# Kernel optimization log

Measured on AMD Instinct MI355X. Metric: run time of the kernel, lower is better.

The kernel has to match this reference:

```python
import jax, jax.numpy as jnp
import numpy as np

COS_EPS = 1e-6      # torch CosineSimilarity eps
NORM_EPS = 1e-12    # F.normalize default eps
NUM_HEADS = 4
TOPK = 5


def setup_inputs() -> dict:
    key = jax.random.key(0)
    ks = jax.random.split(key, 12)
    B, S, D_in, D = 32, 256, 768, 1024
    N = 50000
    sc = 0.02
    return {
        "hidden": jax.random.normal(ks[0], (B, S, D_in), jnp.float32),
        "table": jax.random.normal(ks[1], (N, D), jnp.float32),
        "fc1_w": jax.random.normal(ks[2], (D, D_in), jnp.float32) * sc,
        "fc1_b": jax.random.normal(ks[3], (D,), jnp.float32) * sc,
        "q_w": jax.random.normal(ks[4], (D, D), jnp.float32) * sc,
        "q_b": jax.random.normal(ks[5], (D,), jnp.float32) * sc,
        "k_w": jax.random.normal(ks[6], (D, D), jnp.float32) * sc,
        "k_b": jax.random.normal(ks[7], (D,), jnp.float32) * sc,
        "v_w": jax.random.normal(ks[8], (D, D), jnp.float32) * sc,
        "v_b": jax.random.normal(ks[9], (D,), jnp.float32) * sc,
        "out_w": jax.random.normal(ks[10], (D, D), jnp.float32) * sc,
        "out_b": jax.random.normal(ks[11], (D,), jnp.float32) * sc,
    }


def reference(hidden, table, fc1_w, fc1_b, q_w, q_b, k_w, k_b, v_w, v_b, out_w, out_b):
    B, S, _ = hidden.shape
    D = fc1_w.shape[0]
    H = NUM_HEADS
    hd = D // H

    # fc1 over last BERT hidden states: [B,S,1024]
    x = jnp.einsum("bsi,di->bsd", hidden, fc1_w) + fc1_b

    # ---- per-sample retrieval (vectorized over batch) ----
    m = jnp.mean(x, axis=1)                       # [B,D] mean over seq
    tn = jnp.linalg.norm(table, axis=1)           # [N]
    mn = jnp.linalg.norm(m, axis=1)               # [B]
    sim = (m @ table.T) / (jnp.maximum(mn, COS_EPS)[:, None]
                           * jnp.maximum(tn, COS_EPS)[None, :])  # [B,N]
    best = jnp.argmax(sim, axis=1)                # [B] top-1 cosine match

    tab_n = table / jnp.maximum(tn, NORM_EPS)[:, None]  # L2-normalized table
    sel = tab_n[best]                             # [B,D]
    # squared euclidean distance, expanded form (avoids [B,N,D] intermediate)
    d2 = (jnp.sum(sel * sel, axis=1)[:, None]
          - 2.0 * (sel @ tab_n.T)
          + jnp.sum(tab_n * tab_n, axis=1)[None, :])  # [B,N]
    _, idx = jax.lax.top_k(-d2, TOPK)             # 5 smallest distances
    targets = table[idx]                          # [B,5,D] (unnormalized rows)

    # ---- torch.nn.MultiheadAttention(query=targets, key=x, value=x) ----
    q = (jnp.einsum("bqd,ed->bqe", targets, q_w) + q_b).reshape(B, TOPK, H, hd)
    k = (jnp.einsum("bsd,ed->bse", x, k_w) + k_b).reshape(B, S, H, hd)
    v = (jnp.einsum("bsd,ed->bse", x, v_w) + v_b).reshape(B, S, H, hd)
    scores = jnp.einsum("bqhd,bkhd->bhqk", q, k) / jnp.sqrt(jnp.asarray(hd, x.dtype))
    attn = jax.nn.softmax(scores, axis=-1)        # [B,H,5,S]
    o = jnp.einsum("bhqk,bkhd->bqhd", attn, v).reshape(B, TOPK, D)
    attn_out = jnp.einsum("bqe,de->bqd", o, out_w) + out_b  # [B,5,D]

    return jnp.sum(attn_out, axis=1)              # [B,D]
```

## Files before the change

### kernel.cpp

```cpp
#include <hip/hip_runtime.h>
#include <stdint.h>

typedef short bf16x8 __attribute__((ext_vector_type(8)));
typedef float f32x4 __attribute__((ext_vector_type(4)));

#define NROWS 50000
#define BATCH 32
#define SEQ 256
#define DIN 768
#define DMODEL 1024
#define NTOPK 5
#define DOTS_BLOCKS 782
#define CHUNKF 64
#define NCHUNK (DMODEL / CHUNKF)

__device__ inline unsigned short f2bf(float f) {
  union { float f; unsigned u; } x; x.f = f;
  unsigned u = x.u;
  unsigned r = u + 0x7fffu + ((u >> 16) & 1u);
  return (unsigned short)(r >> 16);
}
__device__ inline float bf2f(unsigned short h) {
  union { unsigned u; float f; } x; x.u = ((unsigned)h) << 16; return x.f;
}

__device__ __forceinline__ void gl_lds16(const void* g, void* l) {
  __builtin_amdgcn_global_load_lds(
      (const __attribute__((address_space(1))) unsigned int*)g,
      (__attribute__((address_space(3))) unsigned int*)l, 16, 0, 0);
}

__global__ void k_f32_to_bf16(const float* __restrict__ in, unsigned short* __restrict__ out, int n) {
  int i = (blockIdx.x * blockDim.x + threadIdx.x) * 4;
  int stride = gridDim.x * blockDim.x * 4;
  for (; i < n; i += stride) {
    float4 f = *(const float4*)(in + i);
    ushort4 o;
    o.x = f2bf(f.x); o.y = f2bf(f.y); o.z = f2bf(f.z); o.w = f2bf(f.w);
    *(ushort4*)(out + i) = o;
  }
}

__global__ void k_f32_to_bf16_3(const float* __restrict__ i0, unsigned short* __restrict__ o0, int n0,
                                const float* __restrict__ i1, unsigned short* __restrict__ o1, int n1,
                                const float* __restrict__ i2, unsigned short* __restrict__ o2, int n2) {
  int base = (blockIdx.x * blockDim.x + threadIdx.x) * 4;
  int stride = gridDim.x * blockDim.x * 4;
  for (int i = base; i < n0; i += stride) {
    float4 f = *(const float4*)(i0 + i);
    ushort4 o; o.x = f2bf(f.x); o.y = f2bf(f.y); o.z = f2bf(f.z); o.w = f2bf(f.w);
    *(ushort4*)(o0 + i) = o;
  }
  for (int i = base; i < n1; i += stride) {
    float4 f = *(const float4*)(i1 + i);
    ushort4 o; o.x = f2bf(f.x); o.y = f2bf(f.y); o.z = f2bf(f.z); o.w = f2bf(f.w);
    *(ushort4*)(o1 + i) = o;
  }
  for (int i = base; i < n2; i += stride) {
    float4 f = *(const float4*)(i2 + i);
    ushort4 o; o.x = f2bf(f.x); o.y = f2bf(f.y); o.z = f2bf(f.z); o.w = f2bf(f.w);
    *(ushort4*)(o2 + i) = o;
  }
}

__global__ void k_mean_part(const float* __restrict__ hidden, float* __restrict__ hpart) {
  int b = blockIdx.x >> 3, tc = blockIdx.x & 7;
  int i = threadIdx.x;
  const float* p = hidden + ((size_t)b * SEQ + tc * 32) * DIN + i;
  float s = 0.f;
  #pragma unroll 4
  for (int t = 0; t < 32; ++t) s += p[t * DIN];
  hpart[((size_t)tc * 32 + b) * DIN + i] = s;
}
__global__ void k_mean_reduce(const float* __restrict__ hpart, float* __restrict__ hm) {
  int b = blockIdx.x;
  int i = threadIdx.x;
  float s = 0.f;
  #pragma unroll
  for (int tc = 0; tc < 8; ++tc) s += hpart[((size_t)tc * 32 + b) * DIN + i];
  hm[b * DIN + i] = s * (1.0f / SEQ);
}

__global__ void k_sgemm_wt(const float* __restrict__ A, const float* __restrict__ W,
                           const float* __restrict__ bias, float* __restrict__ C,
                           int M, int N, int K, float beta) {
  __shared__ float A_l[32][65];
  __shared__ float W_l[64][65];
  int tid = threadIdx.x;
  int tx = tid & 63, ty = tid >> 6;
  int n0 = blockIdx.x * 64, m0 = blockIdx.y * 32;
  float acc[8] = {0.f,0.f,0.f,0.f,0.f,0.f,0.f,0.f};
  for (int k0 = 0; k0 < K; k0 += 64) {
    #pragma unroll
    for (int i = 0; i < 8; ++i) {
      int idx = tid + 256 * i; int r = idx >> 6, c = idx & 63;
      A_l[r][c] = A[(size_t)(m0 + r) * K + k0 + c];
    }
    #pragma unroll
    for (int i = 0; i < 16; ++i) {
      int idx = tid + 256 * i; int r = idx >> 6, c = idx & 63;
      W_l[r][c] = W[(size_t)(n0 + r) * K + k0 + c];
    }
    __syncthreads();
    for (int kk = 0; kk < 64; ++kk) {
      float wv = W_l[tx][kk];
      #pragma unroll
      for (int r = 0; r < 8; ++r) acc[r] += A_l[ty * 8 + r][kk] * wv;
    }
    __syncthreads();
  }
  float bv = bias[n0 + tx] * beta;
  #pragma unroll
  for (int r = 0; r < 8; ++r) C[(size_t)(m0 + ty * 8 + r) * N + n0 + tx] = acc[r] + bv;
}

__global__ __launch_bounds__(256) void k_bf16_gemm(const unsigned short* __restrict__ A,
    const unsigned short* __restrict__ W, const float* __restrict__ bias,
    unsigned short* __restrict__ C, int M, int N, int K) {
  __shared__ unsigned short As[128][32];
  __shared__ unsigned short Ws[128][32];
  int tid = threadIdx.x;
  int wave = tid >> 6, lane = tid & 63;
  int wr = wave >> 1, wc = wave & 1;
  int bm = blockIdx.y * 128, bn = blockIdx.x * 128;
  int srow = lane >> 2;
  int scol = (lane & 3) * 8;
  f32x4 acc[4][4] = {};
  for (int k0 = 0; k0 < K; k0 += 32) {
    #pragma unroll
    for (int j = 0; j < 2; ++j) {
      int r0 = wave * 32 + j * 16;
      gl_lds16(A + (size_t)(bm + r0 + srow) * K + k0 + scol, &As[r0][0]);
      gl_lds16(W + (size_t)(bn + r0 + srow) * K + k0 + scol, &Ws[r0][0]);
    }
    __syncthreads();
    bf16x8 af[4], bfr[4];
    #pragma unroll
    for (int mi = 0; mi < 4; ++mi)
      af[mi] = *(const bf16x8*)(&As[wr * 64 + mi * 16 + (lane & 15)][(lane >> 4) * 8]);
    #pragma unroll
    for (int ni = 0; ni < 4; ++ni)
      bfr[ni] = *(const bf16x8*)(&Ws[wc * 64 + ni * 16 + (lane & 15)][(lane >> 4) * 8]);
    #pragma unroll
    for (int mi = 0; mi < 4; ++mi)
      #pragma unroll
      for (int ni = 0; ni < 4; ++ni)
        acc[mi][ni] = __builtin_amdgcn_mfma_f32_16x16x32_bf16(af[mi], bfr[ni], acc[mi][ni], 0, 0, 0);
    __syncthreads();
  }
  #pragma unroll
  for (int ni = 0; ni < 4; ++ni) {
    int col = bn + wc * 64 + ni * 16 + (lane & 15);
    float bv = bias[col];
    #pragma unroll
    for (int mi = 0; mi < 4; ++mi) {
      #pragma unroll
      for (int j = 0; j < 4; ++j) {
        int row = bm + wr * 64 + mi * 16 + (lane >> 4) * 4 + j;
        C[(size_t)row * N + col] = f2bf(acc[mi][ni][j] + bv);
      }
    }
  }
}

__global__ __launch_bounds__(256, 4) void k_dots(const float* __restrict__ table,
    const float* __restrict__ vecs, float* __restrict__ norm2g,
    float* __restrict__ candv, int* __restrict__ candi, int pass1, float eps) {
  __shared__ float t_lds[2][64 * 64];
  __shared__ float norm_lds[64];
  __shared__ float iv_lds[64];
  float* dot_lds = &t_lds[0][0];

  int tid = threadIdx.x;
  int wave = tid >> 6, lane = tid & 63;
  int rbase = blockIdx.x * 64;

  int b0 = __builtin_amdgcn_readfirstlane(wave * 8);
  const float* qb = vecs + (size_t)b0 * DMODEL;

  int u = lane & 15;
  int rsub = lane >> 4;

  float acc[8] = {0.f,0.f,0.f,0.f,0.f,0.f,0.f,0.f};
  float accn = 0.f;

  auto STAGE = [&](int buf, int k0) {
    #pragma unroll
    for (int j = 0; j < 4; ++j) {
      int rl = wave * 16 + j * 4 + rsub;
      int gr = rbase + rl; if (gr >= NROWS) gr = NROWS - 1;
      int c = ((u & 7) ^ (rl & 7)) | (u & 8);
      gl_lds16(table + (size_t)gr * DMODEL + k0 + c * 4,
               &t_lds[buf][(wave * 16 + j * 4) * 64]);
    }
  };

  STAGE(0, 0);
  __syncthreads();
  int cur = 0;
  for (int ch = 0; ch < NCHUNK; ++ch) {
    int k0 = ch * CHUNKF;
    if (ch + 1 < NCHUNK) STAGE(cur ^ 1, k0 + CHUNKF);
    #pragma unroll 2
    for (int q4 = 0; q4 < 16; ++q4) {
      int uu = ((q4 & 7) ^ (lane & 7)) | (q4 & 8);
      float4 tv = *(const float4*)(&t_lds[cur][lane * 64 + uu * 4]);
      if (pass1 && wave == 0)
        accn += tv.x * tv.x + tv.y * tv.y + tv.z * tv.z + tv.w * tv.w;
      #pragma unroll
      for (int j = 0; j < 8; ++j) {
        float4 qv = *(const float4*)(qb + (size_t)j * DMODEL + k0 + q4 * 4);
        acc[j] += tv.x * qv.x + tv.y * qv.y + tv.z * qv.z + tv.w * qv.w;
      }
    }
    __syncthreads();
    cur ^= 1;
  }

  #pragma unroll
  for (int j = 0; j < 8; ++j) dot_lds[(wave * 8 + j) * 66 + lane] = acc[j];
  if (wave == 0) {
    norm_lds[lane] = accn;
    if (pass1) {
      int rw = rbase + lane;
      if (rw < NROWS) norm2g[rw] = accn;
    }
  }
  __syncthreads();
  if (tid < 64) {
    int rc = rbase + tid;
    if (rc >= NROWS) rc = NROWS - 1;
    float n2 = pass1 ? norm_lds[tid] : norm2g[rc];
    iv_lds[tid] = 1.0f / fmaxf(sqrtf(n2), eps);
  }
  __syncthreads();

  if (tid < 32) {
    float tv[5]; int ti[5];
    #pragma unroll
    for (int j = 0; j < 5; ++j) { tv[j] = -3.4e38f; ti[j] = 0x7fffffff; }
    for (int r = 0; r < 64; ++r) {
      int rw = rbase + r;
      if (rw >= NROWS) break;
      float v = dot_lds[tid * 66 + r] * iv_lds[r];
      if (v > tv[4] || (v == tv[4] && rw < ti[4])) {
        tv[4] = v; ti[4] = rw;
        #pragma unroll
        for (int j = 4; j > 0; --j) {
          bool sw = (tv[j] > tv[j-1]) || (tv[j] == tv[j-1] && ti[j] < ti[j-1]);
          if (sw) {
            float fv = tv[j]; tv[j] = tv[j-1]; tv[j-1] = fv;
            int ivx = ti[j]; ti[j] = ti[j-1]; ti[j-1] = ivx;
          }
        }
      }
    }
    #pragma unroll
    for (int j = 0; j < 5; ++j) {
      candv[((size_t)blockIdx.x * 32 + tid) * 5 + j] = tv[j];
      candi[((size_t)blockIdx.x * 32 + tid) * 5 + j] = ti[j];
    }
  }
}

__global__ void k_merge(const float* __restrict__ candv, const int* __restrict__ candi,
                        int* __restrict__ out_idx, int K, int nblk) {
  int b = blockIdx.x;
  int tid = threadIdx.x;
  float tv[5]; int ti[5];
  #pragma unroll
  for (int j = 0; j < 5; ++j) { tv[j] = -3.4e38f; ti[j] = 0x7fffffff; }
  for (int blk = tid; blk < nblk; blk += 256) {
    #pragma unroll
    for (int j = 0; j < 5; ++j) {
      float v = candv[((size_t)blk * 32 + b) * 5 + j];
      int idx = candi[((size_t)blk * 32 + b) * 5 + j];
      if (v > tv[4] || (v == tv[4] && idx < ti[4])) {
        tv[4] = v; ti[4] = idx;
        #pragma unroll
        for (int jj = 4; jj > 0; --jj) {
          bool sw = (tv[jj] > tv[jj-1]) || (tv[jj] == tv[jj-1] && ti[jj] < ti[jj-1]);
          if (sw) {
            float fv = tv[jj]; tv[jj] = tv[jj-1]; tv[jj-1] = fv;
            int ivx = ti[jj]; ti[jj] = ti[jj-1]; ti[jj-1] = ivx;
          }
        }
      }
    }
  }
  __shared__ float lv[256 * 5];
  __shared__ int   li[256 * 5];
  #pragma unroll
  for (int j = 0; j < 5; ++j) { lv[tid * 5 + j] = tv[j]; li[tid * 5 + j] = ti[j]; }
  __syncthreads();
  for (int off = 128; off >= 1; off >>= 1) {
    if (tid < off) {
      float av[5], bv[5]; int ai[5], bi[5];
      #pragma unroll
      for (int j = 0; j < 5; ++j) {
        av[j] = lv[tid * 5 + j]; ai[j] = li[tid * 5 + j];
        bv[j] = lv[(tid + off) * 5 + j]; bi[j] = li[(tid + off) * 5 + j];
      }
      int pa = 0, pb = 0;
      float mv[5]; int mi[5];
      #pragma unroll
      for (int j = 0; j < 5; ++j) {
        bool ta = (av[pa] > bv[pb]) || (av[pa] == bv[pb] && ai[pa] < bi[pb]);
        if (ta) { mv[j] = av[pa]; mi[j] = ai[pa]; ++pa; }
        else    { mv[j] = bv[pb]; mi[j] = bi[pb]; ++pb; }
      }
      #pragma unroll
      for (int j = 0; j < 5; ++j) { lv[tid * 5 + j] = mv[j]; li[tid * 5 + j] = mi[j]; }
    }
    __syncthreads();
  }
  if (tid == 0) {
    for (int j = 0; j < K; ++j) out_idx[b * K + j] = li[j];
  }
}

__global__ void k_gather_sel(const float* __restrict__ table, const int* __restrict__ best,
                             float* __restrict__ sel) {
  int b = blockIdx.x, e = threadIdx.x;
  int idx = best[b];
  sel[b * DMODEL + e] = table[(size_t)idx * DMODEL + e];
}

__global__ void k_gather_targets(const float* __restrict__ table, const int* __restrict__ idx5,
                                 float* __restrict__ tg) {
  int bt = blockIdx.x, e = threadIdx.x;
  int idx = idx5[bt];
  tg[(size_t)bt * DMODEL + e] = table[(size_t)idx * DMODEL + e];
}

__global__ __launch_bounds__(256) void k_attention(const float* __restrict__ q,
    const unsigned short* __restrict__ kb, const unsigned short* __restrict__ vb,
    float* __restrict__ obuf) {
  int bt = blockIdx.x;
  int b = bt / NTOPK;
  int tid = threadIdx.x;
  __shared__ float q_l[DMODEL];
  __shared__ float sc[4][SEQ];
  #pragma unroll
  for (int j = 0; j < 4; ++j) q_l[tid + 256 * j] = q[(size_t)bt * DMODEL + tid + 256 * j];
  __syncthreads();
  {
    int s = tid;
    const unsigned short* krow = kb + ((size_t)(b * SEQ + s)) * DMODEL;
    #pragma unroll
    for (int h = 0; h < 4; ++h) {
      float d = 0.f;
      for (int dd = 0; dd < 256; dd += 8) {
        uint4 pk = *(const uint4*)(krow + h * 256 + dd);
        const unsigned short* ph = (const unsigned short*)&pk;
        #pragma unroll
        for (int j2 = 0; j2 < 8; ++j2) d += bf2f(ph[j2]) * q_l[h * 256 + dd + j2];
      }
      sc[h][s] = d * 0.0625f;
    }
  }
  __syncthreads();
  {
    int h = tid >> 6, lane = tid & 63;
    float vals[4];
    float mx = -3.4e38f;
    #pragma unroll
    for (int j = 0; j < 4; ++j) { vals[j] = sc[h][lane + 64 * j]; mx = fmaxf(mx, vals[j]); }
    #pragma unroll
    for (int o = 1; o < 64; o <<= 1) mx = fmaxf(mx, __shfl_xor(mx, o));
    float sum = 0.f;
    #pragma unroll
    for (int j = 0; j < 4; ++j) { vals[j] = expf(vals[j] - mx); sum += vals[j]; }
    #pragma unroll
    for (int o = 1; o < 64; o <<= 1) sum += __shfl_xor(sum, o);
    float rz = 1.0f / sum;
    #pragma unroll
    for (int j = 0; j < 4; ++j) sc[h][lane + 64 * j] = vals[j] * rz;
  }
  __syncthreads();
  {
    int h = tid >> 6;
    int e0 = tid * 4;
    float a0 = 0.f, a1 = 0.f, a2 = 0.f, a3 = 0.f;
    const unsigned short* vbase = vb + (size_t)(b * SEQ) * DMODEL + e0;
    for (int s = 0; s < SEQ; ++s) {
      float w = sc[h][s];
      ushort4 v4 = *(const ushort4*)(vbase + (size_t)s * DMODEL);
      a0 += w * bf2f(v4.x); a1 += w * bf2f(v4.y); a2 += w * bf2f(v4.z); a3 += w * bf2f(v4.w);
    }
    float* op = obuf + (size_t)bt * DMODEL + e0;
    op[0] = a0; op[1] = a1; op[2] = a2; op[3] = a3;
  }
}

__global__ void k_osum(const float* __restrict__ obuf, float* __restrict__ osum) {
  int g = blockIdx.x * blockDim.x + threadIdx.x;
  if (g >= BATCH * DMODEL) return;
  int b = g >> 10, e = g & 1023;
  float s = 0.f;
  #pragma unroll
  for (int t = 0; t < NTOPK; ++t) s += obuf[(size_t)(b * NTOPK + t) * DMODEL + e];
  osum[g] = s;
}

extern "C" void kernel_launch(void* const* d_in, const int* in_sizes, int n_in,
                              void* d_out, int out_size, void* d_ws, size_t ws_size,
                              hipStream_t stream) {
  const float* hidden = (const float*)d_in[0];
  const float* table  = (const float*)d_in[1];
  const float* fc1_w  = (const float*)d_in[2];
  const float* fc1_b  = (const float*)d_in[3];
  const float* q_w    = (const float*)d_in[4];
  const float* q_b    = (const float*)d_in[5];
  const float* k_w    = (const float*)d_in[6];
  const float* k_b    = (const float*)d_in[7];
  const float* v_w    = (const float*)d_in[8];
  const float* v_b    = (const float*)d_in[9];
  const float* out_w  = (const float*)d_in[10];
  const float* out_b  = (const float*)d_in[11];
  float* out = (float*)d_out;

  char* ws = (char*)d_ws;
  size_t off = 0;
  auto alloc = [&](size_t bytes) -> void* {
    void* p = ws + off;
    off += (bytes + 255) & ~(size_t)255;
    return p;
  };
  unsigned short* hid_bf  = (unsigned short*)alloc((size_t)BATCH * SEQ * DIN * 2);
  unsigned short* fc1w_bf = (unsigned short*)alloc((size_t)DMODEL * DIN * 2);
  unsigned short* kw_bf   = (unsigned short*)alloc((size_t)DMODEL * DMODEL * 2);
  unsigned short* vw_bf   = (unsigned short*)alloc((size_t)DMODEL * DMODEL * 2);
  unsigned short* x_bf    = (unsigned short*)alloc((size_t)BATCH * SEQ * DMODEL * 2);
  unsigned short* k_bf    = (unsigned short*)alloc((size_t)BATCH * SEQ * DMODEL * 2);
  unsigned short* v_bf    = (unsigned short*)alloc((size_t)BATCH * SEQ * DMODEL * 2);
  float* hpart   = (float*)alloc((size_t)8 * BATCH * DIN * 4);
  float* hm      = (float*)alloc((size_t)BATCH * DIN * 4);
  float* m       = (float*)alloc((size_t)BATCH * DMODEL * 4);
  float* sel     = (float*)alloc((size_t)BATCH * DMODEL * 4);
  float* norm2   = (float*)alloc((size_t)NROWS * 4);
  float* candv   = (float*)alloc((size_t)DOTS_BLOCKS * 32 * 5 * 4);
  int*   candi   = (int*)alloc((size_t)DOTS_BLOCKS * 32 * 5 * 4);
  int*   best    = (int*)alloc(BATCH * 4);
  int*   idx5    = (int*)alloc(BATCH * NTOPK * 4);
  float* targets = (float*)alloc((size_t)BATCH * NTOPK * DMODEL * 4);
  float* qbuf    = (float*)alloc((size_t)BATCH * NTOPK * DMODEL * 4);
  float* obuf    = (float*)alloc((size_t)BATCH * NTOPK * DMODEL * 4);
  float* osum    = (float*)alloc((size_t)BATCH * DMODEL * 4);
  (void)ws_size; (void)in_sizes; (void)n_in; (void)out_size;

  k_f32_to_bf16<<<2048, 256, 0, stream>>>(hidden, hid_bf, BATCH * SEQ * DIN);
  k_f32_to_bf16_3<<<1024, 256, 0, stream>>>(fc1_w, fc1w_bf, DMODEL * DIN,
                                            k_w, kw_bf, DMODEL * DMODEL,
                                            v_w, vw_bf, DMODEL * DMODEL);

  k_mean_part<<<256, 768, 0, stream>>>(hidden, hpart);
  k_mean_reduce<<<32, 768, 0, stream>>>(hpart, hm);
  k_sgemm_wt<<<dim3(16, 1), 256, 0, stream>>>(hm, fc1_w, fc1_b, m, 32, DMODEL, DIN, 1.0f);

  k_bf16_gemm<<<dim3(8, 64), 256, 0, stream>>>(hid_bf, fc1w_bf, fc1_b, x_bf, BATCH * SEQ, DMODEL, DIN);

  k_dots<<<DOTS_BLOCKS, 256, 0, stream>>>(table, m, norm2, candv, candi, 1, 1e-6f);
  k_merge<<<32, 256, 0, stream>>>(candv, candi, best, 1, DOTS_BLOCKS);
  k_gather_sel<<<32, 1024, 0, stream>>>(table, best, sel);

  k_dots<<<DOTS_BLOCKS, 256, 0, stream>>>(table, sel, norm2, candv, candi, 0, 1e-12f);
  k_merge<<<32, 256, 0, stream>>>(candv, candi, idx5, NTOPK, DOTS_BLOCKS);
  k_gather_targets<<<160, 1024, 0, stream>>>(table, idx5, targets);

  k_sgemm_wt<<<dim3(16, 5), 256, 0, stream>>>(targets, q_w, q_b, qbuf, BATCH * NTOPK, DMODEL, DMODEL, 1.0f);

  k_bf16_gemm<<<dim3(8, 64), 256, 0, stream>>>(x_bf, kw_bf, k_b, k_bf, BATCH * SEQ, DMODEL, DMODEL);
  k_bf16_gemm<<<dim3(8, 64), 256, 0, stream>>>(x_bf, vw_bf, v_b, v_bf, BATCH * SEQ, DMODEL, DMODEL);

  k_attention<<<160, 256, 0, stream>>>(qbuf, k_bf, v_bf, obuf);
  k_osum<<<128, 256, 0, stream>>>(obuf, osum);
  k_sgemm_wt<<<dim3(16, 1), 256, 0, stream>>>(osum, out_w, out_b, out, 32, DMODEL, DMODEL, 5.0f);
}
```

Measured before the change: 644.2 us.

## Stage table and query chunks through registers into padded LDS in k_dots

Replaces the async global-to-LDS swizzled loads with register-staged float4 loads written into an LDS tile padded to a 68-float pitch. The query vectors are also staged per chunk into shared memory instead of being read from global memory inside the inner loop. The pipeline becomes load-next into registers, then write to LDS, with a single barrier per chunk. The aim is to cut repeated global and L1 traffic for the query vectors and avoid bank conflicts, at the cost of more registers and LDS, which may lower occupancy under launch_bounds(256,4).

Measured after the change: 790.0 us. +22.6%, slower.

```diff
diff --git a/kernel.cpp b/kernel.cpp
--- a/kernel.cpp
+++ b/kernel.cpp
@@ -11,6 +11,7 @@
 #define DMODEL 1024
 #define NTOPK 5
 #define DOTS_BLOCKS 782
+#define TPITCH 68
 #define CHUNKF 64
 #define NCHUNK (DMODEL / CHUNKF)
 
@@ -166,7 +167,8 @@
 __global__ __launch_bounds__(256, 4) void k_dots(const float* __restrict__ table,
     const float* __restrict__ vecs, float* __restrict__ norm2g,
     float* __restrict__ candv, int* __restrict__ candi, int pass1, float eps) {
-  __shared__ float t_lds[2][64 * 64];
+  __shared__ float t_lds[2][64 * TPITCH];
+  __shared__ float q_lds[4 * 8 * CHUNKF];
   __shared__ float norm_lds[64];
   __shared__ float iv_lds[64];
   float* dot_lds = &t_lds[0][0];
@@ -175,46 +177,55 @@
   int wave = tid >> 6, lane = tid & 63;
   int rbase = blockIdx.x * 64;
 
-  int b0 = __builtin_amdgcn_readfirstlane(wave * 8);
-  const float* qb = vecs + (size_t)b0 * DMODEL;
-
-  int u = lane & 15;
-  int rsub = lane >> 4;
+  int srow = tid >> 2;
+  int sc4 = tid & 3;
+  int grow = rbase + srow;
+  if (grow >= NROWS) grow = NROWS - 1;
+  const float* gsrc = table + (size_t)grow * DMODEL;
+
+  const float* qsrc = vecs + (size_t)(wave * 8 + (lane >> 3)) * DMODEL + (lane & 7) * 8;
+  int qoff = wave * 8 * CHUNKF + (lane >> 3) * CHUNKF + (lane & 7) * 8;
 
   float acc[8] = {0.f,0.f,0.f,0.f,0.f,0.f,0.f,0.f};
   float accn = 0.f;
 
-  auto STAGE = [&](int buf, int k0) {
-    #pragma unroll
-    for (int j = 0; j < 4; ++j) {
-      int rl = wave * 16 + j * 4 + rsub;
-      int gr = rbase + rl; if (gr >= NROWS) gr = NROWS - 1;
-      int c = ((u & 7) ^ (rl & 7)) | (u & 8);
-      gl_lds16(table + (size_t)gr * DMODEL + k0 + c * 4,
-               &t_lds[buf][(wave * 16 + j * 4) * 64]);
-    }
+  float4 treg0, treg1, treg2, treg3, qreg0, qreg1;
+  auto LOAD = [&](int k0) {
+    treg0 = *(const float4*)(gsrc + k0 + (sc4 + 0) * 4);
+    treg1 = *(const float4*)(gsrc + k0 + (sc4 + 4) * 4);
+    treg2 = *(const float4*)(gsrc + k0 + (sc4 + 8) * 4);
+    treg3 = *(const float4*)(gsrc + k0 + (sc4 + 12) * 4);
+    qreg0 = *(const float4*)(qsrc + k0);
+    qreg1 = *(const float4*)(qsrc + k0 + 4);
   };
-
-  STAGE(0, 0);
-  __syncthreads();
-  int cur = 0;
+  auto WRITE = [&](int buf) {
+    *(float4*)(&t_lds[buf][srow * TPITCH + (sc4 + 0) * 4]) = treg0;
+    *(float4*)(&t_lds[buf][srow * TPITCH + (sc4 + 4) * 4]) = treg1;
+    *(float4*)(&t_lds[buf][srow * TPITCH + (sc4 + 8) * 4]) = treg2;
+    *(float4*)(&t_lds[buf][srow * TPITCH + (sc4 + 12) * 4]) = treg3;
+    *(float4*)(&q_lds[qoff]) = qreg0;
+    *(float4*)(&q_lds[qoff + 4]) = qreg1;
+  };
+
+  LOAD(0);
   for (int ch = 0; ch < NCHUNK; ++ch) {
-    int k0 = ch * CHUNKF;
-    if (ch + 1 < NCHUNK) STAGE(cur ^ 1, k0 + CHUNKF);
-    #pragma unroll 2
+    int cur = ch & 1;
+    WRITE(cur);
+    __syncthreads();
+    if (ch + 1 < NCHUNK) LOAD((ch + 1) * CHUNKF);
+    const float* tb = &t_lds[cur][lane * TPITCH];
+    const float* qb = &q_lds[wave * 8 * CHUNKF];
+    #pragma unroll 4
     for (int q4 = 0; q4 < 16; ++q4) {
-      int uu = ((q4 & 7) ^ (lane & 7)) | (q4 & 8);
-      float4 tv = *(const float4*)(&t_lds[cur][lane * 64 + uu * 4]);
+      float4 tv = *(const float4*)(tb + q4 * 4);
       if (pass1 && wave == 0)
         accn += tv.x * tv.x + tv.y * tv.y + tv.z * tv.z + tv.w * tv.w;
       #pragma unroll
       for (int j = 0; j < 8; ++j) {
-        float4 qv = *(const float4*)(qb + (size_t)j * DMODEL + k0 + q4 * 4);
+        float4 qv = *(const float4*)(qb + j * CHUNKF + q4 * 4);
         acc[j] += tv.x * qv.x + tv.y * qv.y + tv.z * qv.z + tv.w * qv.w;
       }
     }
-    __syncthreads();
-    cur ^= 1;
   }
 
   #pragma unroll
```

## Use split-bf16 MFMA for table-query dot products in retrieval kernel

Applied to the files above, without the earlier changes.

Replaces the scalar FP32 FMA dot-product loop in k_dots with bf16 MFMA instructions, using a hi/lo split (3 MFMAs per product) on both the table rows and the query vectors to keep near-FP32 accuracy. Table chunks are now loaded into registers, converted to hi/lo bf16 and written to swizzled LDS, replacing the direct global-to-LDS copies. A new small kernel splits the query vectors, and the row norm is computed by all threads during conversion. The aim is to stop the two 200MB table scans being compute-bound on VALU, at the cost of extra conversion work, more LDS traffic and small precision differences that could flip argmax ties.

Result: faster. 592.5 us (-8.0%).

```diff
diff --git a/kernel.cpp b/kernel.cpp
--- a/kernel.cpp
+++ b/kernel.cpp
@@ -23,6 +23,15 @@
 __device__ inline float bf2f(unsigned short h) {
   union { unsigned u; float f; } x; x.u = ((unsigned)h) << 16; return x.f;
 }
+__device__ inline ushort4 cvt_hi4(float4 f) {
+  ushort4 h; h.x = f2bf(f.x); h.y = f2bf(f.y); h.z = f2bf(f.z); h.w = f2bf(f.w); return h;
+}
+__device__ inline ushort4 cvt_lo4(float4 f, ushort4 h) {
+  ushort4 l;
+  l.x = f2bf(f.x - bf2f(h.x)); l.y = f2bf(f.y - bf2f(h.y));
+  l.z = f2bf(f.z - bf2f(h.z)); l.w = f2bf(f.w - bf2f(h.w));
+  return l;
+}
 
 __device__ __forceinline__ void gl_lds16(const void* g, void* l) {
   __builtin_amdgcn_global_load_lds(
@@ -61,6 +70,17 @@
     ushort4 o; o.x = f2bf(f.x); o.y = f2bf(f.y); o.z = f2bf(f.z); o.w = f2bf(f.w);
     *(ushort4*)(o2 + i) = o;
   }
+}
+
+__global__ void k_split_q(const float* __restrict__ v, unsigned short* __restrict__ qhi,
+                          unsigned short* __restrict__ qlo) {
+  int b = blockIdx.x;
+  int e0 = threadIdx.x * 4;
+  float4 f = *(const float4*)(v + (size_t)b * DMODEL + e0);
+  ushort4 h = cvt_hi4(f);
+  ushort4 l = cvt_lo4(f, h);
+  *(ushort4*)(qhi + (size_t)b * DMODEL + e0) = h;
+  *(ushort4*)(qlo + (size_t)b * DMODEL + e0) = l;
 }
 
 __global__ void k_mean_part(const float* __restrict__ hidden, float* __restrict__ hpart) {
@@ -164,74 +184,107 @@
 }
 
 __global__ __launch_bounds__(256, 4) void k_dots(const float* __restrict__ table,
-    const float* __restrict__ vecs, float* __restrict__ norm2g,
-    float* __restrict__ candv, int* __restrict__ candi, int pass1, float eps) {
-  __shared__ float t_lds[2][64 * 64];
-  __shared__ float norm_lds[64];
+    const unsigned short* __restrict__ qhi, const unsigned short* __restrict__ qlo,
+    float* __restrict__ norm2g, float* __restrict__ candv, int* __restrict__ candi,
+    int pass1, float eps) {
+  __shared__ unsigned short As_hi[2][64 * 64];
+  __shared__ unsigned short As_lo[2][64 * 64];
+  __shared__ float npart[64][4];
   __shared__ float iv_lds[64];
-  float* dot_lds = &t_lds[0][0];
+  float* dot_lds = (float*)&As_hi[0][0];
 
   int tid = threadIdx.x;
   int wave = tid >> 6, lane = tid & 63;
   int rbase = blockIdx.x * 64;
 
-  int b0 = __builtin_amdgcn_readfirstlane(wave * 8);
-  const float* qb = vecs + (size_t)b0 * DMODEL;
-
-  int u = lane & 15;
-  int rsub = lane >> 4;
-
-  float acc[8] = {0.f,0.f,0.f,0.f,0.f,0.f,0.f,0.f};
+  int r = tid >> 2;
+  int q4 = tid & 3;
+  int grow = rbase + r; if (grow >= NROWS) grow = NROWS - 1;
+  const float* gsrc = table + (size_t)grow * DMODEL + q4 * 16;
+  int wslot0 = ((q4 * 2) ^ (r & 7)) * 8;
+  int wslot1 = ((q4 * 2 + 1) ^ (r & 7)) * 8;
+  int wbase = r * 64;
+
+  int abase = (wave * 16 + (lane & 15)) * 64;
+  int al7 = lane & 7;
+  const unsigned short* qh0 = qhi + (size_t)(lane & 15) * DMODEL + (lane >> 4) * 8;
+  const unsigned short* qh1 = qh0 + 16 * DMODEL;
+  const unsigned short* ql0 = qlo + (size_t)(lane & 15) * DMODEL + (lane >> 4) * 8;
+  const unsigned short* ql1 = ql0 + 16 * DMODEL;
+
   float accn = 0.f;
-
-  auto STAGE = [&](int buf, int k0) {
-    #pragma unroll
-    for (int j = 0; j < 4; ++j) {
-      int rl = wave * 16 + j * 4 + rsub;
-      int gr = rbase + rl; if (gr >= NROWS) gr = NROWS - 1;
-      int c = ((u & 7) ^ (rl & 7)) | (u & 8);
-      gl_lds16(table + (size_t)gr * DMODEL + k0 + c * 4,
-               &t_lds[buf][(wave * 16 + j * 4) * 64]);
-    }
+  f32x4 acc0 = {}, acc1 = {};
+  float4 f0, f1, f2, f3;
+
+  auto LOAD = [&](int k0) {
+    f0 = *(const float4*)(gsrc + k0);
+    f1 = *(const float4*)(gsrc + k0 + 4);
+    f2 = *(const float4*)(gsrc + k0 + 8);
+    f3 = *(const float4*)(gsrc + k0 + 12);
   };
-
-  STAGE(0, 0);
-  __syncthreads();
-  int cur = 0;
+  auto WRITE = [&](int buf) {
+    ushort4 h0 = cvt_hi4(f0), h1 = cvt_hi4(f1), h2 = cvt_hi4(f2), h3 = cvt_hi4(f3);
+    ushort4 l0 = cvt_lo4(f0, h0), l1 = cvt_lo4(f1, h1), l2 = cvt_lo4(f2, h2), l3 = cvt_lo4(f3, h3);
+    accn += f0.x*f0.x + f0.y*f0.y + f0.z*f0.z + f0.w*f0.w
+          + f1.x*f1.x + f1.y*f1.y + f1.z*f1.z + f1.w*f1.w
+          + f2.x*f2.x + f2.y*f2.y + f2.z*f2.z + f2.w*f2.w
+          + f3.x*f3.x + f3.y*f3.y + f3.z*f3.z + f3.w*f3.w;
+    *(ushort4*)&As_hi[buf][wbase + wslot0]     = h0;
+    *(ushort4*)&As_hi[buf][wbase + wslot0 + 4] = h1;
+    *(ushort4*)&As_hi[buf][wbase + wslot1]     = h2;
+    *(ushort4*)&As_hi[buf][wbase + wslot1 + 4] = h3;
+    *(ushort4*)&As_lo[buf][wbase + wslot0]     = l0;
+    *(ushort4*)&As_lo[buf][wbase + wslot0 + 4] = l1;
+    *(ushort4*)&As_lo[buf][wbase + wslot1]     = l2;
+    *(ushort4*)&As_lo[buf][wbase + wslot1 + 4] = l3;
+  };
+
+  LOAD(0);
   for (int ch = 0; ch < NCHUNK; ++ch) {
+    int buf = ch & 1;
     int k0 = ch * CHUNKF;
-    if (ch + 1 < NCHUNK) STAGE(cur ^ 1, k0 + CHUNKF);
-    #pragma unroll 2
-    for (int q4 = 0; q4 < 16; ++q4) {
-      int uu = ((q4 & 7) ^ (lane & 7)) | (q4 & 8);
-      float4 tv = *(const float4*)(&t_lds[cur][lane * 64 + uu * 4]);
-      if (pass1 && wave == 0)
-        accn += tv.x * tv.x + tv.y * tv.y + tv.z * tv.z + tv.w * tv.w;
-      #pragma unroll
-      for (int j = 0; j < 8; ++j) {
-        float4 qv = *(const float4*)(qb + (size_t)j * DMODEL + k0 + q4 * 4);
-        acc[j] += tv.x * qv.x + tv.y * qv.y + tv.z * qv.z + tv.w * qv.w;
-      }
-    }
-    __syncthreads();
-    cur ^= 1;
-  }
-
-  #pragma unroll
-  for (int j = 0; j < 8; ++j) dot_lds[(wave * 8 + j) * 66 + lane] = acc[j];
-  if (wave == 0) {
-    norm_lds[lane] = accn;
+    WRITE(buf);
+    if (ch + 1 < NCHUNK) LOAD(k0 + CHUNKF);
+    #pragma unroll
+    for (int kk = 0; kk < 2; ++kk) {
+      int s = ((kk * 4 + (lane >> 4)) ^ al7) * 8;
+      bf16x8 ah = *(const bf16x8*)&As_hi[buf][abase + s];
+      bf16x8 al = *(const bf16x8*)&As_lo[buf][abase + s];
+      int qoff = k0 + kk * 32;
+      bf16x8 bh0 = *(const bf16x8*)(qh0 + qoff);
+      bf16x8 bh1 = *(const bf16x8*)(qh1 + qoff);
+      bf16x8 bl0 = *(const bf16x8*)(ql0 + qoff);
+      bf16x8 bl1 = *(const bf16x8*)(ql1 + qoff);
+      acc0 = __builtin_amdgcn_mfma_f32_16x16x32_bf16(ah, bh0, acc0, 0, 0, 0);
+      acc1 = __builtin_amdgcn_mfma_f32_16x16x32_bf16(ah, bh1, acc1, 0, 0, 0);
+      acc0 = __builtin_amdgcn_mfma_f32_16x16x32_bf16(ah, bl0, acc0, 0, 0, 0);
+      acc1 = __builtin_amdgcn_mfma_f32_16x16x32_bf16(ah, bl1, acc1, 0, 0, 0);
+      acc0 = __builtin_amdgcn_mfma_f32_16x16x32_bf16(al, bh0, acc0, 0, 0, 0);
+      acc1 = __builtin_amdgcn_mfma_f32_16x16x32_bf16(al, bh1, acc1, 0, 0, 0);
+    }
+  }
+
+  npart[r][q4] = accn;
+  __syncthreads();
+  if (tid < 64) {
+    int rw = rbase + tid;
+    int rc = rw < NROWS ? rw : NROWS - 1;
+    float n2;
     if (pass1) {
-      int rw = rbase + lane;
-      if (rw < NROWS) norm2g[rw] = accn;
-    }
-  }
-  __syncthreads();
-  if (tid < 64) {
-    int rc = rbase + tid;
-    if (rc >= NROWS) rc = NROWS - 1;
-    float n2 = pass1 ? norm_lds[tid] : norm2g[rc];
+      n2 = npart[tid][0] + npart[tid][1] + npart[tid][2] + npart[tid][3];
+      if (rw < NROWS) norm2g[rw] = n2;
+    } else {
+      n2 = norm2g[rc];
+    }
     iv_lds[tid] = 1.0f / fmaxf(sqrtf(n2), eps);
+  }
+  __syncthreads();
+  #pragma unroll
+  for (int j = 0; j < 4; ++j) {
+    int row = wave * 16 + (lane >> 4) * 4 + j;
+    float iv = iv_lds[row];
+    dot_lds[(0 * 16 + (lane & 15)) * 66 + row] = acc0[j] * iv;
+    dot_lds[(1 * 16 + (lane & 15)) * 66 + row] = acc1[j] * iv;
   }
   __syncthreads();
 
@@ -239,10 +292,10 @@
     float tv[5]; int ti[5];
     #pragma unroll
     for (int j = 0; j < 5; ++j) { tv[j] = -3.4e38f; ti[j] = 0x7fffffff; }
-    for (int r = 0; r < 64; ++r) {
-      int rw = rbase + r;
+    for (int rr = 0; rr < 64; ++rr) {
+      int rw = rbase + rr;
       if (rw >= NROWS) break;
-      float v = dot_lds[tid * 66 + r] * iv_lds[r];
+      float v = dot_lds[tid * 66 + rr];
       if (v > tv[4] || (v == tv[4] && rw < ti[4])) {
         tv[4] = v; ti[4] = rw;
         #pragma unroll
@@ -434,6 +487,8 @@
   unsigned short* x_bf    = (unsigned short*)alloc((size_t)BATCH * SEQ * DMODEL * 2);
   unsigned short* k_bf    = (unsigned short*)alloc((size_t)BATCH * SEQ * DMODEL * 2);
   unsigned short* v_bf    = (unsigned short*)alloc((size_t)BATCH * SEQ * DMODEL * 2);
+  unsigned short* qhi     = (unsigned short*)alloc((size_t)BATCH * DMODEL * 2);
+  unsigned short* qlo     = (unsigned short*)alloc((size_t)BATCH * DMODEL * 2);
   float* hpart   = (float*)alloc((size_t)8 * BATCH * DIN * 4);
   float* hm      = (float*)alloc((size_t)BATCH * DIN * 4);
   float* m       = (float*)alloc((size_t)BATCH * DMODEL * 4);
@@ -460,11 +515,13 @@
 
   k_bf16_gemm<<<dim3(8, 64), 256, 0, stream>>>(hid_bf, fc1w_bf, fc1_b, x_bf, BATCH * SEQ, DMODEL, DIN);
 
-  k_dots<<<DOTS_BLOCKS, 256, 0, stream>>>(table, m, norm2, candv, candi, 1, 1e-6f);
+  k_split_q<<<32, 256, 0, stream>>>(m, qhi, qlo);
+  k_dots<<<DOTS_BLOCKS, 256, 0, stream>>>(table, qhi, qlo, norm2, candv, candi, 1, 1e-6f);
   k_merge<<<32, 256, 0, stream>>>(candv, candi, best, 1, DOTS_BLOCKS);
   k_gather_sel<<<32, 1024, 0, stream>>>(table, best, sel);
 
-  k_dots<<<DOTS_BLOCKS, 256, 0, stream>>>(table, sel, norm2, candv, candi, 0, 1e-12f);
+  k_split_q<<<32, 256, 0, stream>>>(sel, qhi, qlo);
+  k_dots<<<DOTS_BLOCKS, 256, 0, stream>>>(table, qhi, qlo, norm2, candv, candi, 0, 1e-12f);
   k_merge<<<32, 256, 0, stream>>>(candv, candi, idx5, NTOPK, DOTS_BLOCKS);
   k_gather_targets<<<160, 1024, 0, stream>>>(table, idx5, targets);
 
```
